# Optimization experiments

Hardware: AMD Instinct MI355X
Metric: run time of the kernel (lower is better)

The kernel has to match this reference:

```python
import jax, jax.numpy as jnp
import numpy as np

NT, NP, E, H, DIM = 100000, 50000, 800000, 128, 128


def _lin(key, fi, fo):
    k1, k2 = jax.random.split(key)
    w = jax.random.normal(k1, (fi, fo), jnp.float32) * 0.02
    b = jax.random.normal(k2, (fo,), jnp.float32) * 0.02
    return w, b


def _conv_params(key, d_src, d_dst, d_out):
    ks = jax.random.split(key, 5)
    Wq, bq = _lin(ks[0], d_dst, d_out)
    Wk, bk = _lin(ks[1], d_src, d_out)
    Wv, bv = _lin(ks[2], d_src, d_out)
    Ws, bs = _lin(ks[3], d_dst, d_out)
    Wb = jax.random.normal(ks[4], (3 * d_out, 1), jnp.float32) * 0.02
    return Wq, bq, Wk, bk, Wv, bv, Ws, bs, Wb


def setup_inputs() -> dict:
    key = jax.random.key(0)
    ks = jax.random.split(key, 12)
    inp = {}
    inp['x_token'] = jax.random.normal(ks[0], (NT, 1), jnp.float32)
    inp['x_phrase'] = jax.random.normal(ks[1], (NP, H), jnp.float32)
    inp['W_emb'], inp['b_emb'] = _lin(ks[2], 1, H)
    (inp['Wq_tp'], inp['bq_tp'], inp['Wk_tp'], inp['bk_tp'], inp['Wv_tp'],
     inp['bv_tp'], inp['Ws_tp'], inp['bs_tp'], inp['Wb_tp']) = _conv_params(ks[3], H, H, H)
    (inp['Wq_pt'], inp['bq_pt'], inp['Wk_pt'], inp['bk_pt'], inp['Wv_pt'],
     inp['bv_pt'], inp['Ws_pt'], inp['bs_pt'], inp['Wb_pt']) = _conv_params(ks[4], H, H, H)
    inp['W_head'], inp['b_head'] = _lin(ks[5], H, DIM)
    inp['src_tp'] = jax.random.randint(ks[6], (E,), 0, NT, jnp.int32)
    inp['dst_tp'] = jax.random.randint(ks[7], (E,), 0, NP, jnp.int32)
    inp['src_pt'] = jax.random.randint(ks[8], (E,), 0, NP, jnp.int32)
    inp['dst_pt'] = jax.random.randint(ks[9], (E,), 0, NT, jnp.int32)
    return inp


def _tconv(x_src, x_dst, src, dst, Wq, bq, Wk, bk, Wv, bv, Ws, bs, Wb):
    # PyG TransformerConv, heads=1, beta=True, eval mode (no dropout).
    n_dst = x_dst.shape[0]
    d = Wq.shape[1]
    q = x_dst @ Wq + bq          # [Ndst, d]
    k = x_src @ Wk + bk          # [Nsrc, d]
    v = x_src @ Wv + bv          # [Nsrc, d]
    scores = jnp.sum(q[dst] * k[src], axis=-1) / jnp.sqrt(jnp.float32(d))  # [E]
    m = jax.ops.segment_max(scores, dst, num_segments=n_dst)
    m = jnp.where(jnp.isfinite(m), m, 0.0)  # nodes with no in-edges
    e = jnp.exp(scores - m[dst])
    denom = jax.ops.segment_sum(e, dst, num_segments=n_dst)
    alpha = e / (denom[dst] + 1e-16)                       # segment softmax over dst
    out = jax.ops.segment_sum(alpha[:, None] * v[src], dst, num_segments=n_dst)
    skip = x_dst @ Ws + bs
    beta = jax.nn.sigmoid(jnp.concatenate([out, skip, out - skip], axis=-1) @ Wb)
    return beta * skip + (1.0 - beta) * out


def _forward(x_token, x_phrase, W_emb, b_emb,
             Wq_tp, bq_tp, Wk_tp, bk_tp, Wv_tp, bv_tp, Ws_tp, bs_tp, Wb_tp,
             Wq_pt, bq_pt, Wk_pt, bk_pt, Wv_pt, bv_pt, Ws_pt, bs_pt, Wb_pt,
             W_head, b_head, src_tp, dst_tp, src_pt, dst_pt):
    h_t = x_token @ W_emb + b_emb   # [NT, H]
    h_p = x_phrase                  # [NP, H]
    # conv1 (HeteroConv aggr='sum'; each node type has exactly one incoming edge type)
    p1 = _tconv(h_t, h_p, src_tp, dst_tp, Wq_tp, bq_tp, Wk_tp, bk_tp, Wv_tp, bv_tp, Ws_tp, bs_tp, Wb_tp)
    t1 = _tconv(h_p, h_t, src_pt, dst_pt, Wq_pt, bq_pt, Wk_pt, bk_pt, Wv_pt, bv_pt, Ws_pt, bs_pt, Wb_pt)
    p1 = jax.nn.leaky_relu(p1, 0.01)
    t1 = jax.nn.leaky_relu(t1, 0.01)
    # conv2 shares the SAME conv modules (same params). Only the token output is used downstream.
    t2 = _tconv(p1, t1, src_pt, dst_pt, Wq_pt, bq_pt, Wk_pt, bk_pt, Wv_pt, bv_pt, Ws_pt, bs_pt, Wb_pt)
    return t2 @ W_head + b_head     # [NT, DIM]


def reference(x_token, x_phrase, W_emb, b_emb, Wq_tp, bq_tp, Wk_tp, bk_tp, Wv_tp, bv_tp, Ws_tp, bs_tp, Wb_tp, Wq_pt, bq_pt, Wk_pt, bk_pt, Wv_pt, bv_pt, Ws_pt, bs_pt, Wb_pt, W_head, b_head, src_tp, dst_tp, src_pt, dst_pt):
    return _forward(x_token, x_phrase, W_emb, b_emb,
                    Wq_tp, bq_tp, Wk_tp, bk_tp, Wv_tp, bv_tp, Ws_tp, bs_tp, Wb_tp,
                    Wq_pt, bq_pt, Wk_pt, bk_pt, Wv_pt, bv_pt, Ws_pt, bs_pt, Wb_pt,
                    W_head, b_head, src_tp, dst_tp, src_pt, dst_pt)
```

## Files before the change

### kernel.cpp

```cpp
#include <hip/hip_runtime.h>
#include <math.h>

#define NT 100000
#define NP 50000
#define NE 800000
#define H 128
#define NB 196
#define BCAP 8192

#define CDIV(a,b) (((a)+(b)-1)/(b))

typedef __attribute__((ext_vector_type(8))) short s16x8;
typedef __attribute__((ext_vector_type(4))) short s16x4;
typedef __attribute__((ext_vector_type(4))) unsigned short u16x4;
typedef __attribute__((ext_vector_type(4))) float f32x4;

static __device__ __forceinline__ float dot4(float4 a, float4 b){
  return a.x*b.x + a.y*b.y + a.z*b.z + a.w*b.w;
}
static __device__ __forceinline__ float b2f(unsigned short u){
  union { unsigned int i; float f; } c; c.i = ((unsigned int)u) << 16; return c.f;
}
static __device__ __forceinline__ unsigned short f2b(float f){
  union { float f; unsigned int i; } c; c.f = f;
  unsigned int x = c.i;
  unsigned int r = (x + 0x7fffu + ((x >> 16) & 1u)) >> 16;
  return (unsigned short)r;
}
static __device__ __forceinline__ float4 cvt4u(u16x4 h){
  return make_float4(b2f(h[0]), b2f(h[1]), b2f(h[2]), b2f(h[3]));
}

__global__ void kvec4(const float* __restrict__ e, const float* __restrict__ be,
    const float* W0, const float* bi0, float* u0, float* w0,
    const float* W1, const float* bi1, float* u1, float* w1,
    const float* W2, const float* bi2, float* u2, float* w2,
    const float* W3, const float* bi3, float* u3, float* w3){
  const float *W, *bi; float *u, *w;
  switch (blockIdx.x){
    case 0: W=W0; bi=bi0; u=u0; w=w0; break;
    case 1: W=W1; bi=bi1; u=u1; w=w1; break;
    case 2: W=W2; bi=bi2; u=u2; w=w2; break;
    default:W=W3; bi=bi3; u=u3; w=w3; break;
  }
  int j = threadIdx.x;
  float su = 0.f, sw = 0.f;
  for (int i = 0; i < H; ++i) {
    float wv = W[i*H + j];
    su += e[i]*wv;
    sw += be[i]*wv;
  }
  u[j] = su;
  w[j] = sw + bi[j];
}

__global__ void ksetup(const float* __restrict__ Wq, const float* __restrict__ Wk,
                       const float* __restrict__ bq, float* __restrict__ Wqk,
                       float* __restrict__ bqk){
  int i = blockIdx.x;
  int m = threadIdx.x;
  __shared__ float wqr[H];
  wqr[m] = Wq[i*H + m];
  __syncthreads();
  const float* wkr = Wk + m*H;
  float s = 0.f;
  for (int j = 0; j < H; ++j) s += wqr[j] * wkr[j];
  Wqk[i*H + m] = s;
  if (i == 0){
    float t = 0.f;
    for (int j = 0; j < H; ++j) t += bq[j] * wkr[j];
    bqk[m] = t;
  }
}
__global__ void kvqb(const float* __restrict__ Wq, const float* __restrict__ bq,
                     const float* __restrict__ bk, float* __restrict__ vqb,
                     float* __restrict__ c0){
  int i = threadIdx.x;
  float s = 0.f;
  for (int j = 0; j < H; ++j) s += Wq[i*H + j]*bk[j];
  vqb[i] = s;
  if (i == 0){
    float t = 0.f;
    for (int j = 0; j < H; ++j) t += bq[j]*bk[j];
    *c0 = t;
  }
}

__global__ void kprep(const float* W0, unsigned short* P0,
                      const float* W1, unsigned short* P1,
                      const float* W2, unsigned short* P2,
                      const float* W3, unsigned short* P3,
                      const float* W4, unsigned short* P4,
                      const float* W5, unsigned short* P5,
                      const float* W6, unsigned short* P6){
  const float* W; unsigned short* P;
  switch (blockIdx.x){
    case 0: W=W0; P=P0; break;
    case 1: W=W1; P=P1; break;
    case 2: W=W2; P=P2; break;
    case 3: W=W3; P=P3; break;
    case 4: W=W4; P=P4; break;
    case 5: W=W5; P=P5; break;
    default:W=W6; P=P6; break;
  }
  int tid = threadIdx.x;
  for (int it = 0; it < 16; ++it){
    int gid = it*256 + tid;
    int n  = gid & 127;
    int kg = gid >> 7;
    int k0 = kg*4;
    float w0 = W[(k0+0)*H + n];
    float w1 = W[(k0+1)*H + n];
    float w2 = W[(k0+2)*H + n];
    float w3 = W[(k0+3)*H + n];
    unsigned short h0=f2b(w0), h1=f2b(w1), h2=f2b(w2), h3=f2b(w3);
    s16x4 hv; hv[0]=(short)h0; hv[1]=(short)h1; hv[2]=(short)h2; hv[3]=(short)h3;
    s16x4 lv; lv[0]=(short)f2b(w0-b2f(h0)); lv[1]=(short)f2b(w1-b2f(h1));
              lv[2]=(short)f2b(w2-b2f(h2)); lv[3]=(short)f2b(w3-b2f(h3));
    int base = n*128 + (((kg>>1) ^ (n&15))<<3) + ((kg&1)<<2);
    *(s16x4*)(P + base) = hv;
    *(s16x4*)(P + 16384 + base) = lv;
  }
}

static __device__ __forceinline__ void stage_pre32_512(const unsigned short* __restrict__ Wpre,
    unsigned short* __restrict__ WH, int tid){
  const s16x8* src = (const s16x8*)Wpre;
  s16x8 tmp[4];
  #pragma unroll
  for (int it = 0; it < 4; ++it) tmp[it] = src[it*512 + tid];
  #pragma unroll
  for (int it = 0; it < 4; ++it) *(s16x8*)(WH + (it*512 + tid)*8) = tmp[it];
}

static __device__ __forceinline__ void mfma_passW2(const s16x8 AH[4], const s16x8 AL[4],
    const unsigned short* __restrict__ WH, int l15, int l4, f32x4 acc[8]){
  #pragma unroll
  for (int t = 0; t < 8; ++t){ acc[t][0]=0.f; acc[t][1]=0.f; acc[t][2]=0.f; acc[t][3]=0.f; }
  #pragma unroll
  for (int s = 0; s < 4; ++s){
    #pragma unroll
    for (int t = 0; t < 8; ++t){
      int n = t*16 + l15;
      int off = n*128 + (((s*4 + l4) ^ l15)<<3);
      s16x8 BH = *(const s16x8*)(WH + off);
      acc[t] = __builtin_amdgcn_mfma_f32_16x16x32_bf16(AH[s], BH, acc[t], 0,0,0);
      acc[t] = __builtin_amdgcn_mfma_f32_16x16x32_bf16(AL[s], BH, acc[t], 0,0,0);
    }
  }
}
static __device__ __forceinline__ void mfma_passW1(const s16x8 AH[4],
    const unsigned short* __restrict__ WH, int l15, int l4, f32x4 acc[8]){
  #pragma unroll
  for (int t = 0; t < 8; ++t){ acc[t][0]=0.f; acc[t][1]=0.f; acc[t][2]=0.f; acc[t][3]=0.f; }
  #pragma unroll
  for (int s = 0; s < 4; ++s){
    #pragma unroll
    for (int t = 0; t < 8; ++t){
      int n = t*16 + l15;
      int off = n*128 + (((s*4 + l4) ^ l15)<<3);
      s16x8 BH = *(const s16x8*)(WH + off);
      acc[t] = __builtin_amdgcn_mfma_f32_16x16x32_bf16(AH[s], BH, acc[t], 0,0,0);
    }
  }
}

static __device__ __forceinline__ void load_aw_f32(const float* __restrict__ X, int M,
    int rowb, int l15, int l4, s16x8 AH[4], s16x8 AL[4]){
  int row = rowb + l15;
  const float* xr = X + (size_t)row*H;
  bool ok = row < M;
  #pragma unroll
  for (int s = 0; s < 4; ++s){
    int kb = s*32 + l4*8;
    float4 f0 = ok ? *(const float4*)(xr+kb)   : make_float4(0.f,0.f,0.f,0.f);
    float4 f1 = ok ? *(const float4*)(xr+kb+4) : make_float4(0.f,0.f,0.f,0.f);
    float xs[8] = {f0.x,f0.y,f0.z,f0.w,f1.x,f1.y,f1.z,f1.w};
    s16x8 h, lo;
    #pragma unroll
    for (int e = 0; e < 8; ++e){
      unsigned short hh = f2b(xs[e]);
      h[e]  = (short)hh;
      lo[e] = (short)f2b(xs[e] - b2f(hh));
    }
    AH[s] = h; AL[s] = lo;
  }
}
static __device__ __forceinline__ void load_aw_bf16(const unsigned short* __restrict__ Xb, int M,
    int rowb, int l15, int l4, s16x8 AH[4]){
  int row = rowb + l15;
  const unsigned short* xr = Xb + (size_t)row*H;
  bool ok = row < M;
  #pragma unroll
  for (int s = 0; s < 4; ++s){
    s16x8 h = {0,0,0,0,0,0,0,0};
    if (ok) h = *(const s16x8*)(xr + s*32 + l4*8);
    AH[s] = h;
  }
}

static __device__ __forceinline__ void dots_epiW(const f32x4 (&acc)[8],
    const float* __restrict__ bias, const float* __restrict__ uvec,
    const float* __restrict__ wvec, float2* __restrict__ acout,
    int rowb, int M, int l15, int l4){
  float ub[8], wb[8], bb[8];
  #pragma unroll
  for (int t=0;t<8;++t){ ub[t]=uvec[t*16+l15]; wb[t]=wvec[t*16+l15]; bb[t]=bias[t*16+l15]; }
  #pragma unroll
  for (int r=0;r<4;++r){
    float pa=0.f, pc=0.f;
    #pragma unroll
    for (int t=0;t<8;++t){ float y=acc[t][r]+bb[t]; pa+=y*ub[t]; pc+=y*wb[t]; }
    #pragma unroll
    for (int o=1;o<16;o<<=1){ pa+=__shfl_xor(pa,o); pc+=__shfl_xor(pc,o); }
    int row = rowb + l4*4 + r;
    if (l15==0 && row<M) acout[row]=make_float2(pa,pc);
  }
}

static __device__ __forceinline__ void store_cw_bf16(unsigned short* __restrict__ Y,
    const f32x4 (&acc)[8], const float* __restrict__ bias,
    int rowb, int M, int l15, int l4){
  float bb[8];
  #pragma unroll
  for (int t=0;t<8;++t) bb[t]=bias[t*16+l15];
  #pragma unroll
  for (int r=0;r<4;++r){
    int row = rowb + l4*4 + r;
    if (row < M){
      unsigned short* dr = Y + (size_t)row*H;
      #pragma unroll
      for (int t=0;t<8;++t) dr[t*16+l15] = f2b(acc[t][r] + bb[t]);
    }
  }
}
static __device__ __forceinline__ void store_cw_f32(float* __restrict__ Y,
    const f32x4 (&acc)[8], const float* __restrict__ bias,
    int rowb, int M, int l15, int l4){
  float bb[8];
  #pragma unroll
  for (int t=0;t<8;++t) bb[t]=bias[t*16+l15];
  #pragma unroll
  for (int r=0;r<4;++r){
    int row = rowb + l4*4 + r;
    if (row < M){
      float* dr = Y + (size_t)row*H;
      #pragma unroll
      for (int t=0;t<8;++t) dr[t*16+l15] = acc[t][r] + bb[t];
    }
  }
}

__launch_bounds__(512)
__global__ void k_ph(const float* __restrict__ X, int M,
    const unsigned short* __restrict__ WqP, const float* __restrict__ bq,
    const float* __restrict__ uk, const float* __restrict__ wk, float2* __restrict__ ac1,
    const unsigned short* __restrict__ WsP, const float* __restrict__ bs, unsigned short* __restrict__ S1b,
    const unsigned short* __restrict__ WkP, const float* __restrict__ bk,
    const float* __restrict__ uq, const float* __restrict__ wq, float2* __restrict__ ac2,
    const unsigned short* __restrict__ WvP, const float* __restrict__ bv, unsigned short* __restrict__ Vb){
  __shared__ __align__(16) unsigned short WH[16384];
  int tid=threadIdx.x, lane=tid&63, w=tid>>6, l15=lane&15, l4=lane>>4;
  int rowb = blockIdx.x*128 + w*16;

  s16x8 AH[4], AL[4];
  load_aw_f32(X, M, rowb, l15, l4, AH, AL);

  f32x4 acc[8];
  stage_pre32_512(WqP, WH, tid); __syncthreads();
  mfma_passW2(AH, AL, WH, l15, l4, acc);
  __syncthreads();
  dots_epiW(acc, bq, uk, wk, ac1, rowb, M, l15, l4);

  stage_pre32_512(WsP, WH, tid); __syncthreads();
  mfma_passW2(AH, AL, WH, l15, l4, acc);
  __syncthreads();
  store_cw_bf16(S1b, acc, bs, rowb, M, l15, l4);

  stage_pre32_512(WkP, WH, tid); __syncthreads();
  mfma_passW2(AH, AL, WH, l15, l4, acc);
  __syncthreads();
  dots_epiW(acc, bk, uq, wq, ac2, rowb, M, l15, l4);

  stage_pre32_512(WvP, WH, tid); __syncthreads();
  mfma_passW2(AH, AL, WH, l15, l4, acc);
  store_cw_bf16(Vb, acc, bv, rowb, M, l15, l4);
}

__launch_bounds__(512)
__global__ void k_t3(const unsigned short* __restrict__ T1b, int M,
    const unsigned short* __restrict__ WqkP, const float* __restrict__ bqk,
    unsigned short* __restrict__ qkb,
    const float* __restrict__ vqb, const float* __restrict__ c0,
    float* __restrict__ qbf,
    const unsigned short* __restrict__ WsP, const float* __restrict__ bs,
    unsigned short* __restrict__ Sb){
  __shared__ __align__(16) unsigned short WH[16384];
  int tid=threadIdx.x, lane=tid&63, w=tid>>6, l15=lane&15, l4=lane>>4;
  int rowb = blockIdx.x*128 + w*16;

  s16x8 AH[4];
  load_aw_bf16(T1b, M, rowb, l15, l4, AH);

  float cc0 = *c0;
  {
    float p = 0.f;
    #pragma unroll
    for (int s = 0; s < 4; ++s){
      #pragma unroll
      for (int e = 0; e < 8; ++e)
        p += b2f((unsigned short)AH[s][e]) * vqb[s*32 + l4*8 + e];
    }
    p += __shfl_xor(p, 16);
    p += __shfl_xor(p, 32);
    int row = rowb + l15;
    if (l4 == 0 && row < M) qbf[row] = p + cc0;
  }

  f32x4 acc[8];
  stage_pre32_512(WqkP, WH, tid); __syncthreads();
  mfma_passW1(AH, WH, l15, l4, acc);
  __syncthreads();
  store_cw_bf16(qkb, acc, bqk, rowb, M, l15, l4);

  stage_pre32_512(WsP, WH, tid); __syncthreads();
  mfma_passW1(AH, WH, l15, l4, acc);
  store_cw_bf16(Sb, acc, bs, rowb, M, l15, l4);
}

__launch_bounds__(512)
__global__ void k_cmbh(const unsigned short* __restrict__ Opre, int M,
    const unsigned short* __restrict__ PV2, const float* __restrict__ bv,
    const unsigned short* __restrict__ Sb, const float* __restrict__ Wb,
    const int* __restrict__ deg,
    const unsigned short* __restrict__ PHD, const float* __restrict__ bh,
    float* __restrict__ out){
  __shared__ __align__(16) unsigned short WH[16384];
  __shared__ __align__(16) unsigned short SLDS[128][136];
  int tid=threadIdx.x, lane=tid&63, w=tid>>6, l15=lane&15, l4=lane>>4;
  int row0 = blockIdx.x*128;
  int rowb = row0 + w*16;

  s16x8 AH[4];
  load_aw_bf16(Opre, M, rowb, l15, l4, AH);

  stage_pre32_512(PV2, WH, tid); __syncthreads();
  f32x4 acc[8];
  mfma_passW1(AH, WH, l15, l4, acc);

  {
    float bvv[8], wbA[8], wbB[8], wbC[8];
    #pragma unroll
    for (int t = 0; t < 8; ++t){
      int col = t*16 + l15;
      bvv[t] = bv[col];
      wbA[t] = Wb[col]; wbB[t] = Wb[H + col]; wbC[t] = Wb[2*H + col];
    }
    #pragma unroll
    for (int r = 0; r < 4; ++r){
      int rl = w*16 + l4*4 + r;
      int row = row0 + rl;
      bool ok = row < M;
      float bsc = (ok && deg[row] > 0) ? 1.f : 0.f;
      const unsigned short* sr = Sb + (size_t)(ok ? row : 0)*H;
      float o[8], sk[8];
      float part = 0.f;
      #pragma unroll
      for (int t = 0; t < 8; ++t){
        o[t] = acc[t][r] + bvv[t]*bsc;
        sk[t] = ok ? b2f(sr[t*16 + l15]) : 0.f;
        part += o[t]*wbA[t] + sk[t]*wbB[t] + (o[t]-sk[t])*wbC[t];
      }
      #pragma unroll
      for (int of = 1; of < 16; of <<= 1) part += __shfl_xor(part, of);
      float beta = 1.f/(1.f + __expf(-part));
      #pragma unroll
      for (int t = 0; t < 8; ++t){
        float vv = beta*sk[t] + (1.f-beta)*o[t];
        SLDS[rl][t*16 + l15] = f2b(vv);
      }
    }
  }
  __syncthreads();

  s16x8 A2[4];
  {
    int rl = w*16 + l15;
    #pragma unroll
    for (int s = 0; s < 4; ++s)
      A2[s] = *(const s16x8*)&SLDS[rl][s*32 + l4*8];
  }
  stage_pre32_512(PHD, WH, tid);
  __syncthreads();

  f32x4 a2[8];
  mfma_passW1(A2, WH, l15, l4, a2);
  store_cw_f32(out, a2, bh, rowb, M, l15, l4);
}

template<int GATHER>
__launch_bounds__(256)
__global__ void passA(const int* __restrict__ dst, const int* __restrict__ src,
                      const float* __restrict__ xv, int shift,
                      int* __restrict__ bcnt, int2* __restrict__ out, int n){
  __shared__ int hist[NB];
  __shared__ int base[NB];
  __shared__ int cur[NB];
  int tid = threadIdx.x;
  for (int i = tid; i < NB; i += 256){ hist[i]=0; cur[i]=0; }
  __syncthreads();
  int e0 = blockIdx.x*2048;
  int d[8], s[8];
  #pragma unroll
  for (int k = 0; k < 8; ++k){
    int i = e0 + k*256 + tid;
    if (i < n){ d[k] = dst[i]; s[k] = src[i]; }
    else d[k] = -1;
  }
  #pragma unroll
  for (int k = 0; k < 8; ++k)
    if (d[k] >= 0) atomicAdd(&hist[d[k]>>shift], 1);
  __syncthreads();
  for (int b = tid; b < NB; b += 256)
    base[b] = hist[b] ? atomicAdd(&bcnt[b], hist[b]) : 0;
  __syncthreads();
  #pragma unroll
  for (int k = 0; k < 8; ++k){
    if (d[k] >= 0){
      int b = d[k] >> shift;
      int loc = atomicAdd(&cur[b], 1);
      int2 rec;
      if constexpr (GATHER) rec.x = __float_as_int(xv[s[k]]);
      else                  rec.x = s[k];
      rec.y = d[k] - (b << shift);
      out[(size_t)b*BCAP + base[b] + loc] = rec;
    }
  }
}

__launch_bounds__(512)
__global__ void passB_ph(const int* __restrict__ bcnt, const int2* __restrict__ sorted,
                         const float2* __restrict__ ac, float2* __restrict__ dsv, int np){
  __shared__ float2 acl[256];
  __shared__ float accx[256];
  __shared__ float accy[256];
  int b = blockIdx.x, tid = threadIdx.x;
  int p0 = b*256;
  if (tid < 256){
    int p = p0 + tid;
    acl[tid] = (p < np) ? ac[p] : make_float2(0.f,0.f);
    accx[tid] = 0.f; accy[tid] = 0.f;
  }
  __syncthreads();
  int n = bcnt[b];
  const int2* e = sorted + (size_t)b*BCAP;
  const float RS = 0.08838834764831845f;
  for (int i = tid; i < n; i += 512){
    int2 ed = e[i];
    float x = __int_as_float(ed.x);
    float2 a = acl[ed.y];
    float ex = __expf((x*a.x + a.y)*RS);
    atomicAdd(&accx[ed.y], ex);
    atomicAdd(&accy[ed.y], ex*x);
  }
  __syncthreads();
  if (tid < 256){
    int p = p0 + tid;
    if (p < np) dsv[p] = make_float2(accx[tid], accy[tid]);
  }
}

__launch_bounds__(512)
__global__ void passB_tok(const int* __restrict__ bcnt, const int2* __restrict__ sorted,
                          int* __restrict__ rowptr, int* __restrict__ deg,
                          int* __restrict__ srcs, int ntok){
  __shared__ int cnt[512];
  __shared__ int scn[512];
  __shared__ int cur[512];
  int b = blockIdx.x, tid = threadIdx.x;
  cnt[tid] = 0; cur[tid] = 0;
  __syncthreads();
  int n = bcnt[b];
  const int2* e = sorted + (size_t)b*BCAP;
  for (int i = tid; i < n; i += 512) atomicAdd(&cnt[e[i].y], 1);
  __syncthreads();
  int myc = cnt[tid];
  scn[tid] = myc;
  __syncthreads();
  for (int off = 1; off < 512; off <<= 1){
    int u = (tid >= off) ? scn[tid-off] : 0;
    __syncthreads();
    scn[tid] += u;
    __syncthreads();
  }
  int excl = scn[tid] - myc;
  int tok = b*512 + tid;
  if (tok < ntok){ rowptr[tok] = b*BCAP + excl; deg[tok] = myc; }
  __syncthreads();
  cnt[tid] = excl;
  __syncthreads();
  for (int i = tid; i < n; i += 512){
    int2 ed = e[i];
    int pos = cnt[ed.y] + atomicAdd(&cur[ed.y], 1);
    srcs[(size_t)b*BCAP + pos] = ed.x;
  }
}

template<int OB>
static __device__ __forceinline__ void beta_combine(float4 o, float4 sk,
    const float* __restrict__ Wb, int lane, bool leaky, void* __restrict__ dstRow){
  float4 wb0 = *(const float4*)&Wb[lane*4];
  float4 wb1 = *(const float4*)&Wb[H   + lane*4];
  float4 wb2 = *(const float4*)&Wb[2*H + lane*4];
  float4 dv = make_float4(o.x-sk.x, o.y-sk.y, o.z-sk.z, o.w-sk.w);
  float part = dot4(o,wb0) + dot4(sk,wb1) + dot4(dv,wb2);
  #pragma unroll
  for (int off=1; off<32; off<<=1) part += __shfl_xor(part, off);
  float beta = 1.f/(1.f + __expf(-part));
  float4 r;
  r.x = beta*sk.x + (1.f-beta)*o.x;
  r.y = beta*sk.y + (1.f-beta)*o.y;
  r.z = beta*sk.z + (1.f-beta)*o.z;
  r.w = beta*sk.w + (1.f-beta)*o.w;
  if (leaky){
    r.x = r.x>0.f? r.x : 0.01f*r.x;
    r.y = r.y>0.f? r.y : 0.01f*r.y;
    r.z = r.z>0.f? r.z : 0.01f*r.z;
    r.w = r.w>0.f? r.w : 0.01f*r.w;
  }
  if constexpr (OB){
    ushort4 h; h.x=f2b(r.x); h.y=f2b(r.y); h.z=f2b(r.z); h.w=f2b(r.w);
    *(ushort4*)((unsigned short*)dstRow + lane*4) = h;
  } else {
    *(float4*)((float*)dstRow + lane*4) = r;
  }
}

static __device__ __forceinline__ void beta_combine16(const float o[8], const float sk[8],
    const float* __restrict__ Wb, int lane, bool leaky, unsigned short* __restrict__ dstRow){
  float part = 0.f;
  #pragma unroll
  for (int e = 0; e < 8; ++e){
    int col = lane*8 + e;
    part += o[e]*Wb[col] + sk[e]*Wb[H+col] + (o[e]-sk[e])*Wb[2*H+col];
  }
  #pragma unroll
  for (int off = 1; off < 16; off <<= 1) part += __shfl_xor(part, off);
  float beta = 1.f/(1.f + __expf(-part));
  s16x8 h;
  #pragma unroll
  for (int e = 0; e < 8; ++e){
    float r = beta*sk[e] + (1.f-beta)*o[e];
    if (leaky) r = r > 0.f ? r : 0.01f*r;
    h[e] = (short)f2b(r);
  }
  __builtin_nontemporal_store(h, (s16x8*)(dstRow + lane*8));
}

__global__ void kcomb1(const float2* __restrict__ dsv,
                       const float* __restrict__ uv, const float* __restrict__ wv,
                       const unsigned short* __restrict__ S, const float* __restrict__ Wb,
                       unsigned short* __restrict__ out, int n){
  int gid = (blockIdx.x*blockDim.x + threadIdx.x) >> 5;
  int lane = threadIdx.x & 31;
  if (gid >= n) return;
  float2 ds = dsv[gid];
  float d = ds.x, sv = ds.y;
  float inv = 1.f/(d + 1e-16f);
  float4 u4 = *(const float4*)&uv[lane*4];
  float4 w4 = *(const float4*)&wv[lane*4];
  float4 o = make_float4((sv*u4.x + d*w4.x)*inv, (sv*u4.y + d*w4.y)*inv,
                         (sv*u4.z + d*w4.z)*inv, (sv*u4.w + d*w4.w)*inv);
  u16x4 sh4 = __builtin_nontemporal_load((const u16x4*)(S + (size_t)gid*H + lane*4));
  float4 sk = cvt4u(sh4);
  beta_combine<1>(o, sk, Wb, lane, true, out + (size_t)gid*H);
}

__global__ void knode2(const float* __restrict__ x_tok, const float2* __restrict__ ac,
                       const unsigned short* __restrict__ Vb,
                       const int* __restrict__ rowptr, const int* __restrict__ deg,
                       const int* __restrict__ srcs,
                       const float* __restrict__ us, const float* __restrict__ ws,
                       const float* __restrict__ Wb, unsigned short* __restrict__ out, int n){
  int gid = (blockIdx.x*blockDim.x + threadIdx.x) >> 4;
  int lane = threadIdx.x & 15;
  if (gid >= n) return;
  float xt = x_tok[gid];
  int rp = rowptr[gid], dg = deg[gid];
  const float RS = 0.08838834764831845f;
  float d = 0.f;
  float acc[8] = {0.f,0.f,0.f,0.f,0.f,0.f,0.f,0.f};
  for (int i0 = 0; i0 < dg; i0 += 16){
    int nrem = dg - i0; if (nrem > 16) nrem = 16;
    int mySp = 0; float myE = 0.f;
    if (lane < nrem){
      mySp = srcs[rp + i0 + lane];
      float2 a = ac[mySp];
      myE = __expf((xt*a.x + a.y)*RS);
    }
    float cd = myE;
    #pragma unroll
    for (int of = 1; of < 16; of <<= 1) cd += __shfl_xor(cd, of);
    d += cd;
    int j = 0;
    for (; j+2 <= nrem; j += 2){
      int spA = __shfl(mySp, j, 16),  spB = __shfl(mySp, j+1, 16);
      float eA = __shfl(myE, j, 16),  eB = __shfl(myE, j+1, 16);
      s16x8 hA = *(const s16x8*)(Vb + (size_t)spA*H + lane*8);
      s16x8 hB = *(const s16x8*)(Vb + (size_t)spB*H + lane*8);
      #pragma unroll
      for (int e = 0; e < 8; ++e)
        acc[e] += eA*b2f((unsigned short)hA[e]) + eB*b2f((unsigned short)hB[e]);
    }
    if (j < nrem){
      int sp = __shfl(mySp, j, 16);
      float e0 = __shfl(myE, j, 16);
      s16x8 hv = *(const s16x8*)(Vb + (size_t)sp*H + lane*8);
      #pragma unroll
      for (int e = 0; e < 8; ++e) acc[e] += e0*b2f((unsigned short)hv[e]);
    }
  }
  float inv = 1.f/(d + 1e-16f);
  float o[8], sk[8];
  #pragma unroll
  for (int e = 0; e < 8; ++e){
    int col = lane*8 + e;
    o[e]  = acc[e]*inv;
    sk[e] = xt*us[col] + ws[col];
  }
  beta_combine16(o, sk, Wb, lane, true, out + (size_t)gid*H);
}

__global__ void knode3n(const unsigned short* __restrict__ qkb, const float* __restrict__ qbf,
                        const unsigned short* __restrict__ P1b,
                        const int* __restrict__ rowptr, const int* __restrict__ deg,
                        const int* __restrict__ srcs,
                        unsigned short* __restrict__ Opre, int n){
  int gid = (blockIdx.x*blockDim.x + threadIdx.x) >> 4;
  int lane = threadIdx.x & 15;
  if (gid >= n) return;
  float q[8];
  {
    s16x8 qh = __builtin_nontemporal_load((const s16x8*)(qkb + (size_t)gid*H + lane*8));
    #pragma unroll
    for (int e = 0; e < 8; ++e) q[e] = b2f((unsigned short)qh[e]);
  }
  float qb = qbf[gid];
  int rp = rowptr[gid], dg = deg[gid];
  const float RS = 0.08838834764831845f;
  float d = 0.f;
  float acc[8] = {0.f,0.f,0.f,0.f,0.f,0.f,0.f,0.f};
  int i = 0;
  for (; i+2 <= dg; i += 2){
    int spA = srcs[rp+i], spB = srcs[rp+i+1];
    s16x8 hA = *(const s16x8*)(P1b + (size_t)spA*H + lane*8);
    s16x8 hB = *(const s16x8*)(P1b + (size_t)spB*H + lane*8);
    float pA[8], pB[8];
    float psA = 0.f, psB = 0.f;
    #pragma unroll
    for (int e = 0; e < 8; ++e){
      pA[e] = b2f((unsigned short)hA[e]);
      pB[e] = b2f((unsigned short)hB[e]);
      psA += q[e]*pA[e];
      psB += q[e]*pB[e];
    }
    #pragma unroll
    for (int off=1; off<16; off<<=1){ psA += __shfl_xor(psA,off); psB += __shfl_xor(psB,off); }
    float eA = __expf((psA + qb)*RS), eB = __expf((psB + qb)*RS);
    d += eA + eB;
    #pragma unroll
    for (int e = 0; e < 8; ++e) acc[e] += eA*pA[e] + eB*pB[e];
  }
  if (i < dg){
    int sp = srcs[rp+i];
    s16x8 h = *(const s16x8*)(P1b + (size_t)sp*H + lane*8);
    float p[8];
    float ps = 0.f;
    #pragma unroll
    for (int e = 0; e < 8; ++e){ p[e] = b2f((unsigned short)h[e]); ps += q[e]*p[e]; }
    #pragma unroll
    for (int off=1; off<16; off<<=1) ps += __shfl_xor(ps,off);
    float ex = __expf((ps + qb)*RS);
    d += ex;
    #pragma unroll
    for (int e = 0; e < 8; ++e) acc[e] += ex*p[e];
  }
  float inv = 1.f/(d + 1e-16f);
  s16x8 hres;
  #pragma unroll
  for (int e = 0; e < 8; ++e) hres[e] = (short)f2b(acc[e]*inv);
  __builtin_nontemporal_store(hres, (s16x8*)(Opre + (size_t)gid*H + lane*8));
}

extern "C" void kernel_launch(void* const* d_in, const int* in_sizes, int n_in,
                              void* d_out, int out_size, void* d_ws, size_t ws_size,
                              hipStream_t stream){
  const float* x_token  = (const float*)d_in[0];
  const float* x_phrase = (const float*)d_in[1];
  const float* W_emb    = (const float*)d_in[2];
  const float* b_emb    = (const float*)d_in[3];
  const float* Wq_tp = (const float*)d_in[4];  const float* bq_tp = (const float*)d_in[5];
  const float* Wk_tp = (const float*)d_in[6];  const float* bk_tp = (const float*)d_in[7];
  const float* Wv_tp = (const float*)d_in[8];  const float* bv_tp = (const float*)d_in[9];
  const float* Ws_tp = (const float*)d_in[10]; const float* bs_tp = (const float*)d_in[11];
  const float* Wb_tp = (const float*)d_in[12];
  const float* Wq_pt = (const float*)d_in[13]; const float* bq_pt = (const float*)d_in[14];
  const float* Wk_pt = (const float*)d_in[15]; const float* bk_pt = (const float*)d_in[16];
  const float* Wv_pt = (const float*)d_in[17]; const float* bv_pt = (const float*)d_in[18];
  const float* Ws_pt = (const float*)d_in[19]; const float* bs_pt = (const float*)d_in[20];
  const float* Wb_pt = (const float*)d_in[21];
  const float* W_head = (const float*)d_in[22]; const float* b_head = (const float*)d_in[23];
  const int* src_tp = (const int*)d_in[24];
  const int* dst_tp = (const int*)d_in[25];
  const int* src_pt = (const int*)d_in[26];
  const int* dst_pt = (const int*)d_in[27];
  float* out = (float*)d_out;

  char* base = (char*)d_ws;
  size_t off = 0;
  auto AB = [&](size_t bytes)->void*{ void* p=(void*)(base+off); off += (bytes+15)&~(size_t)15; return p; };
  unsigned short* S1b = (unsigned short*)AB((size_t)NP*H*2);
  unsigned short* P1b = (unsigned short*)AB((size_t)NP*H*2);
  unsigned short* VQ  = (unsigned short*)AB((size_t)NT*H*2);
  unsigned short* Sb  = (unsigned short*)AB((size_t)NT*H*2);
  unsigned short* T1b = (unsigned short*)AB((size_t)NT*H*2);
  unsigned short* qkb = (unsigned short*)AB((size_t)NT*H*2);
  unsigned short* Vb   = VQ;
  unsigned short* Opre = VQ;
  float* qbf = (float*)AB((size_t)NT*4);
  float* Wqk = (float*)AB((size_t)H*H*4);
  float* bqk = (float*)AB((size_t)H*4);
  float* vqb = (float*)AB((size_t)H*4);
  float* c0  = (float*)AB(16);
  unsigned short* PQ1 = (unsigned short*)AB(32768*2);
  unsigned short* PS1 = (unsigned short*)AB(32768*2);
  unsigned short* PK2 = (unsigned short*)AB(32768*2);
  unsigned short* PV2 = (unsigned short*)AB(32768*2);
  unsigned short* PS3 = (unsigned short*)AB(32768*2);
  unsigned short* PHD = (unsigned short*)AB(32768*2);
  unsigned short* PQK = (unsigned short*)AB(32768*2);
  float* vecs = (float*)AB(8*H*4);
  float* uk1=vecs, *wk1=vecs+H, *uv1=vecs+2*H, *wv1=vecs+3*H;
  float* uq2=vecs+4*H, *wq2=vecs+5*H, *us2=vecs+6*H, *ws2=vecs+7*H;
  float2* ac1  = (float2*)AB((size_t)NP*8);
  float2* ac2  = (float2*)AB((size_t)NP*8);
  float2* dsv2 = (float2*)AB((size_t)NP*8);
  int2* sortedP = (int2*)AB((size_t)NB*BCAP*8);
  int2* sortedT = (int2*)AB((size_t)NB*BCAP*8);
  int*  srcsT   = (int*)AB((size_t)NB*BCAP*4);
  int* rowT = (int*)AB((size_t)NT*4);
  int* degT = (int*)AB((size_t)NT*4);
  int* bcnt = (int*)AB((size_t)2*NB*4);
  int* bcntP = bcnt, * bcntT = bcnt + NB;
  (void)ws_size; (void)in_sizes; (void)n_in; (void)out_size;

  const int gP = CDIV(NP,128), gT = CDIV(NT,128);
  const int nbA = CDIV(NE,2048);

  kvec4<<<4,H,0,stream>>>(W_emb, b_emb,
      Wk_tp, bk_tp, uk1, wk1,
      Wv_tp, bv_tp, uv1, wv1,
      Wq_pt, bq_pt, uq2, wq2,
      Ws_pt, bs_pt, us2, ws2);
  ksetup<<<H,H,0,stream>>>(Wq_pt, Wk_pt, bq_pt, Wqk, bqk);
  kvqb<<<1,H,0,stream>>>(Wq_pt, bq_pt, bk_pt, vqb, c0);
  kprep<<<7,256,0,stream>>>(Wq_tp, PQ1, Ws_tp, PS1, Wk_pt, PK2, Wv_pt, PV2,
                            Ws_pt, PS3, W_head, PHD, Wqk, PQK);

  (void)hipMemsetAsync(bcnt, 0, (size_t)2*NB*4, stream);
  passA<1><<<nbA,256,0,stream>>>(dst_tp, src_tp, x_token, 8, bcntP, sortedP, NE);
  passA<0><<<nbA,256,0,stream>>>(dst_pt, src_pt, nullptr, 9, bcntT, sortedT, NE);
  passB_tok<<<NB,512,0,stream>>>(bcntT, sortedT, rowT, degT, srcsT, NT);

  k_ph<<<gP,512,0,stream>>>(x_phrase, NP,
      PQ1, bq_tp, uk1, wk1, ac1,
      PS1, bs_tp, S1b,
      PK2, bk_pt, uq2, wq2, ac2,
      PV2, bv_pt, Vb);

  passB_ph<<<NB,512,0,stream>>>(bcntP, sortedP, ac1, dsv2, NP);
  kcomb1<<<CDIV(NP*32,256),256,0,stream>>>(dsv2, uv1, wv1, S1b, Wb_tp, P1b, NP);

  knode2<<<CDIV(NT*16,256),256,0,stream>>>(x_token, ac2, Vb, rowT, degT, srcsT,
                                           us2, ws2, Wb_pt, T1b, NT);

  k_t3<<<gT,512,0,stream>>>(T1b, NT, PQK, bqk, qkb, vqb, c0, qbf,
                            PS3, bs_pt, Sb);
  knode3n<<<CDIV(NT*16,256),256,0,stream>>>(qkb, qbf, P1b, rowT, degT, srcsT,
                                            Opre, NT);
  k_cmbh<<<gT,512,0,stream>>>(Opre, NT, PV2, bv_pt, Sb, Wb_pt, degT,
                              PHD, b_head, out);
}
```

Baseline: 255.6 us.

## Fuse final token-side GEMMs, edge attention gather, and head into one kernel

Merges k_t3, knode3n and k_cmbh into a single kernel, k_t3f, that works on 128-row blocks. The q/k projection, query bias, attention gather-softmax over neighbours, V projection, skip projection, beta gating and head GEMM all run inside it, with intermediates kept in LDS and registers. This removes the global round trips for qkb, qbf, Sb and Opre, and two launches. The cost is that the irregular gather now runs inside a 512-thread block with heavy LDS use, where each 16-lane group serially handles 4 rows, so occupancy and latency hiding may drop compared with the standalone gather kernel.

```diff
diff --git a/kernel.cpp b/kernel.cpp
--- a/kernel.cpp
+++ b/kernel.cpp
@@ -288,72 +288,146 @@
 }
 
 __launch_bounds__(512)
-__global__ void k_t3(const unsigned short* __restrict__ T1b, int M,
-    const unsigned short* __restrict__ WqkP, const float* __restrict__ bqk,
-    unsigned short* __restrict__ qkb,
+__global__ void k_t3f(const unsigned short* __restrict__ T1b, int M,
+    const unsigned short* __restrict__ PQK, const float* __restrict__ bqk,
     const float* __restrict__ vqb, const float* __restrict__ c0,
-    float* __restrict__ qbf,
-    const unsigned short* __restrict__ WsP, const float* __restrict__ bs,
-    unsigned short* __restrict__ Sb){
-  __shared__ __align__(16) unsigned short WH[16384];
-  int tid=threadIdx.x, lane=tid&63, w=tid>>6, l15=lane&15, l4=lane>>4;
-  int rowb = blockIdx.x*128 + w*16;
-
-  s16x8 AH[4];
-  load_aw_bf16(T1b, M, rowb, l15, l4, AH);
-
-  float cc0 = *c0;
-  {
-    float p = 0.f;
-    #pragma unroll
-    for (int s = 0; s < 4; ++s){
-      #pragma unroll
-      for (int e = 0; e < 8; ++e)
-        p += b2f((unsigned short)AH[s][e]) * vqb[s*32 + l4*8 + e];
-    }
-    p += __shfl_xor(p, 16);
-    p += __shfl_xor(p, 32);
-    int row = rowb + l15;
-    if (l4 == 0 && row < M) qbf[row] = p + cc0;
-  }
-
-  f32x4 acc[8];
-  stage_pre32_512(WqkP, WH, tid); __syncthreads();
-  mfma_passW1(AH, WH, l15, l4, acc);
-  __syncthreads();
-  store_cw_bf16(qkb, acc, bqk, rowb, M, l15, l4);
-
-  stage_pre32_512(WsP, WH, tid); __syncthreads();
-  mfma_passW1(AH, WH, l15, l4, acc);
-  store_cw_bf16(Sb, acc, bs, rowb, M, l15, l4);
-}
-
-__launch_bounds__(512)
-__global__ void k_cmbh(const unsigned short* __restrict__ Opre, int M,
+    const unsigned short* __restrict__ PS3, const float* __restrict__ bs3,
+    const unsigned short* __restrict__ P1b,
+    const int* __restrict__ rowptr, const int* __restrict__ deg,
+    const int* __restrict__ srcs,
     const unsigned short* __restrict__ PV2, const float* __restrict__ bv,
-    const unsigned short* __restrict__ Sb, const float* __restrict__ Wb,
-    const int* __restrict__ deg,
+    const float* __restrict__ Wb,
     const unsigned short* __restrict__ PHD, const float* __restrict__ bh,
     float* __restrict__ out){
   __shared__ __align__(16) unsigned short WH[16384];
   __shared__ __align__(16) unsigned short SLDS[128][136];
+  __shared__ float qbl[128];
   int tid=threadIdx.x, lane=tid&63, w=tid>>6, l15=lane&15, l4=lane>>4;
+  int g = tid>>4, gl = tid&15;
   int row0 = blockIdx.x*128;
   int rowb = row0 + w*16;
+  const float RS = 0.08838834764831845f;
 
   s16x8 AH[4];
-  load_aw_bf16(Opre, M, rowb, l15, l4, AH);
-
-  stage_pre32_512(PV2, WH, tid); __syncthreads();
-  f32x4 acc[8];
-  mfma_passW1(AH, WH, l15, l4, acc);
+  load_aw_bf16(T1b, M, rowb, l15, l4, AH);
 
   {
-    float bvv[8], wbA[8], wbB[8], wbC[8];
+    float cc0 = *c0;
+    float p = 0.f;
+    #pragma unroll
+    for (int s = 0; s < 4; ++s){
+      #pragma unroll
+      for (int e = 0; e < 8; ++e)
+        p += b2f((unsigned short)AH[s][e]) * vqb[s*32 + l4*8 + e];
+    }
+    p += __shfl_xor(p, 16);
+    p += __shfl_xor(p, 32);
+    if (l4 == 0) qbl[w*16 + l15] = p + cc0;
+  }
+
+  stage_pre32_512(PQK, WH, tid);
+  __syncthreads();
+  {
+    f32x4 acc[8];
+    mfma_passW1(AH, WH, l15, l4, acc);
+    float bb[8];
+    #pragma unroll
+    for (int t=0;t<8;++t) bb[t] = bqk[t*16+l15];
+    #pragma unroll
+    for (int r=0;r<4;++r){
+      int rl = w*16 + l4*4 + r;
+      #pragma unroll
+      for (int t=0;t<8;++t) SLDS[rl][t*16+l15] = f2b(acc[t][r] + bb[t]);
+    }
+  }
+  __syncthreads();
+
+  stage_pre32_512(PS3, WH, tid);
+
+  #pragma unroll
+  for (int tk = 0; tk < 4; ++tk){
+    int rl = g*4 + tk;
+    int row = row0 + rl;
+    if (row < M){
+      float q[8];
+      {
+        s16x8 qh = *(const s16x8*)&SLDS[rl][gl*8];
+        #pragma unroll
+        for (int e = 0; e < 8; ++e) q[e] = b2f((unsigned short)qh[e]);
+      }
+      float qb = qbl[rl];
+      int rp = rowptr[row], dg = deg[row];
+      float d = 0.f;
+      float acc8[8] = {0.f,0.f,0.f,0.f,0.f,0.f,0.f,0.f};
+      int i = 0;
+      for (; i+2 <= dg; i += 2){
+        int spA = srcs[rp+i], spB = srcs[rp+i+1];
+        s16x8 hA = *(const s16x8*)(P1b + (size_t)spA*H + gl*8);
+        s16x8 hB = *(const s16x8*)(P1b + (size_t)spB*H + gl*8);
+        float pA[8], pB[8];
+        float psA = 0.f, psB = 0.f;
+        #pragma unroll
+        for (int e = 0; e < 8; ++e){
+          pA[e] = b2f((unsigned short)hA[e]);
+          pB[e] = b2f((unsigned short)hB[e]);
+          psA += q[e]*pA[e];
+          psB += q[e]*pB[e];
+        }
+        #pragma unroll
+        for (int off=1; off<16; off<<=1){ psA += __shfl_xor(psA,off); psB += __shfl_xor(psB,off); }
+        float eA = __expf((psA + qb)*RS), eB = __expf((psB + qb)*RS);
+        d += eA + eB;
+        #pragma unroll
+        for (int e = 0; e < 8; ++e) acc8[e] += eA*pA[e] + eB*pB[e];
+      }
+      if (i < dg){
+        int sp = srcs[rp+i];
+        s16x8 h = *(const s16x8*)(P1b + (size_t)sp*H + gl*8);
+        float p[8];
+        float ps = 0.f;
+        #pragma unroll
+        for (int e = 0; e < 8; ++e){ p[e] = b2f((unsigned short)h[e]); ps += q[e]*p[e]; }
+        #pragma unroll
+        for (int off=1; off<16; off<<=1) ps += __shfl_xor(ps,off);
+        float ex = __expf((ps + qb)*RS);
+        d += ex;
+        #pragma unroll
+        for (int e = 0; e < 8; ++e) acc8[e] += ex*p[e];
+      }
+      float inv = 1.f/(d + 1e-16f);
+      s16x8 hres;
+      #pragma unroll
+      for (int e = 0; e < 8; ++e) hres[e] = (short)f2b(acc8[e]*inv);
+      *(s16x8*)&SLDS[rl][gl*8] = hres;
+    } else {
+      s16x8 z = {0,0,0,0,0,0,0,0};
+      *(s16x8*)&SLDS[rl][gl*8] = z;
+    }
+  }
+  __syncthreads();
+
+  f32x4 skacc[8];
+  mfma_passW1(AH, WH, l15, l4, skacc);
+  s16x8 A2[4];
+  {
+    int rl = w*16 + l15;
+    #pragma unroll
+    for (int s = 0; s < 4; ++s)
+      A2[s] = *(const s16x8*)&SLDS[rl][s*32 + l4*8];
+  }
+  __syncthreads();
+
+  stage_pre32_512(PV2, WH, tid);
+  __syncthreads();
+
+  {
+    f32x4 oacc[8];
+    mfma_passW1(A2, WH, l15, l4, oacc);
+    float bvv[8], bsv[8], wbA[8], wbB[8], wbC[8];
     #pragma unroll
     for (int t = 0; t < 8; ++t){
       int col = t*16 + l15;
-      bvv[t] = bv[col];
+      bvv[t] = bv[col]; bsv[t] = bs3[col];
       wbA[t] = Wb[col]; wbB[t] = Wb[H + col]; wbC[t] = Wb[2*H + col];
     }
     #pragma unroll
@@ -362,13 +436,12 @@
       int row = row0 + rl;
       bool ok = row < M;
       float bsc = (ok && deg[row] > 0) ? 1.f : 0.f;
-      const unsigned short* sr = Sb + (size_t)(ok ? row : 0)*H;
       float o[8], sk[8];
       float part = 0.f;
       #pragma unroll
       for (int t = 0; t < 8; ++t){
-        o[t] = acc[t][r] + bvv[t]*bsc;
-        sk[t] = ok ? b2f(sr[t*16 + l15]) : 0.f;
+        o[t]  = oacc[t][r] + bvv[t]*bsc;
+        sk[t] = skacc[t][r] + bsv[t];
         part += o[t]*wbA[t] + sk[t]*wbB[t] + (o[t]-sk[t])*wbC[t];
       }
       #pragma unroll
@@ -383,19 +456,19 @@
   }
   __syncthreads();
 
-  s16x8 A2[4];
+  s16x8 A3[4];
   {
     int rl = w*16 + l15;
     #pragma unroll
     for (int s = 0; s < 4; ++s)
-      A2[s] = *(const s16x8*)&SLDS[rl][s*32 + l4*8];
+      A3[s] = *(const s16x8*)&SLDS[rl][s*32 + l4*8];
   }
   stage_pre32_512(PHD, WH, tid);
   __syncthreads();
 
-  f32x4 a2[8];
-  mfma_passW1(A2, WH, l15, l4, a2);
-  store_cw_f32(out, a2, bh, rowb, M, l15, l4);
+  f32x4 hacc[8];
+  mfma_passW1(A3, WH, l15, l4, hacc);
+  store_cw_f32(out, hacc, bh, rowb, M, l15, l4);
 }
 
 template<int GATHER>
@@ -629,67 +702,6 @@
     sk[e] = xt*us[col] + ws[col];
   }
   beta_combine16(o, sk, Wb, lane, true, out + (size_t)gid*H);
-}
-
-__global__ void knode3n(const unsigned short* __restrict__ qkb, const float* __restrict__ qbf,
-                        const unsigned short* __restrict__ P1b,
-                        const int* __restrict__ rowptr, const int* __restrict__ deg,
-                        const int* __restrict__ srcs,
-                        unsigned short* __restrict__ Opre, int n){
-  int gid = (blockIdx.x*blockDim.x + threadIdx.x) >> 4;
-  int lane = threadIdx.x & 15;
-  if (gid >= n) return;
-  float q[8];
-  {
-    s16x8 qh = __builtin_nontemporal_load((const s16x8*)(qkb + (size_t)gid*H + lane*8));
-    #pragma unroll
-    for (int e = 0; e < 8; ++e) q[e] = b2f((unsigned short)qh[e]);
-  }
-  float qb = qbf[gid];
-  int rp = rowptr[gid], dg = deg[gid];
-  const float RS = 0.08838834764831845f;
-  float d = 0.f;
-  float acc[8] = {0.f,0.f,0.f,0.f,0.f,0.f,0.f,0.f};
-  int i = 0;
-  for (; i+2 <= dg; i += 2){
-    int spA = srcs[rp+i], spB = srcs[rp+i+1];
-    s16x8 hA = *(const s16x8*)(P1b + (size_t)spA*H + lane*8);
-    s16x8 hB = *(const s16x8*)(P1b + (size_t)spB*H + lane*8);
-    float pA[8], pB[8];
-    float psA = 0.f, psB = 0.f;
-    #pragma unroll
-    for (int e = 0; e < 8; ++e){
-      pA[e] = b2f((unsigned short)hA[e]);
-      pB[e] = b2f((unsigned short)hB[e]);
-      psA += q[e]*pA[e];
-      psB += q[e]*pB[e];
-    }
-    #pragma unroll
-    for (int off=1; off<16; off<<=1){ psA += __shfl_xor(psA,off); psB += __shfl_xor(psB,off); }
-    float eA = __expf((psA + qb)*RS), eB = __expf((psB + qb)*RS);
-    d += eA + eB;
-    #pragma unroll
-    for (int e = 0; e < 8; ++e) acc[e] += eA*pA[e] + eB*pB[e];
-  }
-  if (i < dg){
-    int sp = srcs[rp+i];
-    s16x8 h = *(const s16x8*)(P1b + (size_t)sp*H + lane*8);
-    float p[8];
-    float ps = 0.f;
-    #pragma unroll
-    for (int e = 0; e < 8; ++e){ p[e] = b2f((unsigned short)h[e]); ps += q[e]*p[e]; }
-    #pragma unroll
-    for (int off=1; off<16; off<<=1) ps += __shfl_xor(ps,off);
-    float ex = __expf((ps + qb)*RS);
-    d += ex;
-    #pragma unroll
-    for (int e = 0; e < 8; ++e) acc[e] += ex*p[e];
-  }
-  float inv = 1.f/(d + 1e-16f);
-  s16x8 hres;
-  #pragma unroll
-  for (int e = 0; e < 8; ++e) hres[e] = (short)f2b(acc[e]*inv);
-  __builtin_nontemporal_store(hres, (s16x8*)(Opre + (size_t)gid*H + lane*8));
 }
 
 extern "C" void kernel_launch(void* const* d_in, const int* in_sizes, int n_in,
@@ -721,13 +733,8 @@
   auto AB = [&](size_t bytes)->void*{ void* p=(void*)(base+off); off += (bytes+15)&~(size_t)15; return p; };
   unsigned short* S1b = (unsigned short*)AB((size_t)NP*H*2);
   unsigned short* P1b = (unsigned short*)AB((size_t)NP*H*2);
-  unsigned short* VQ  = (unsigned short*)AB((size_t)NT*H*2);
-  unsigned short* Sb  = (unsigned short*)AB((size_t)NT*H*2);
+  unsigned short* Vb  = (unsigned short*)AB((size_t)NP*H*2);
   unsigned short* T1b = (unsigned short*)AB((size_t)NT*H*2);
-  unsigned short* qkb = (unsigned short*)AB((size_t)NT*H*2);
-  unsigned short* Vb   = VQ;
-  unsigned short* Opre = VQ;
-  float* qbf = (float*)AB((size_t)NT*4);
   float* Wqk = (float*)AB((size_t)H*H*4);
   float* bqk = (float*)AB((size_t)H*4);
   float* vqb = (float*)AB((size_t)H*4);
@@ -784,10 +791,10 @@
   knode2<<<CDIV(NT*16,256),256,0,stream>>>(x_token, ac2, Vb, rowT, degT, srcsT,
                                            us2, ws2, Wb_pt, T1b, NT);
 
-  k_t3<<<gT,512,0,stream>>>(T1b, NT, PQK, bqk, qkb, vqb, c0, qbf,
-                            PS3, bs_pt, Sb);
-  knode3n<<<CDIV(NT*16,256),256,0,stream>>>(qkb, qbf, P1b, rowT, degT, srcsT,
-                                            Opre, NT);
-  k_cmbh<<<gT,512,0,stream>>>(Opre, NT, PV2, bv_pt, Sb, Wb_pt, degT,
-                              PHD, b_head, out);
-}
+  k_t3f<<<gT,512,0,stream>>>(T1b, NT,
+      PQK, bqk, vqb, c0,
+      PS3, bs_pt,
+      P1b, rowT, degT, srcsT,
+      PV2, bv_pt, Wb_pt,
+      PHD, b_head, out);
+}
```

Measured after the change: 246.2 us. -3.7%, faster.
